# Performance work log

Measured on AMD Instinct MI355X. Metric: run time of the kernel, lower is better.

Reference implementation:

```python
import jax, jax.numpy as jnp
import numpy as np


def setup_inputs() -> dict:
    key = jax.random.key(0)
    k1, k2 = jax.random.split(key)
    B, S, H, D = 4, 2048, 12, 64
    v = jax.random.normal(k1, (B, S, H, D), dtype=jnp.float32)
    # learned per-head positional weights, sorted ascending along last dim
    # (mirrors torch.sort(torch.randn(H, S), dim=-1)[0])
    w = jnp.sort(jax.random.normal(k2, (H, S), dtype=jnp.float32), axis=-1)
    return {"v": v, "w": w}


def reference(v, w):
    # PositionalBias._naive
    # v: [B, S, H, D]; w: [H, S_max]
    B, S, H, D = v.shape
    seq_len = S - 2  # v[:, 1:-1] is the non-special-token span
    w_ = w[:, :seq_len]  # [H, seq_len]
    # _construct_bias builds bias[h, l, j] = w[h, |l - j|] (symmetric Toeplitz)
    pos = jnp.arange(seq_len)
    idx = jnp.abs(pos[:, None] - pos[None, :])  # [seq_len, seq_len]
    bias = w_[:, idx]  # [H, seq_len, seq_len]
    # zero-pad one row/col on each side -> [H, S, S]
    bias = jnp.pad(bias, ((0, 0), (1, 1), (1, 1)))
    # z_pb: [1, S, H]
    z_pb = jnp.sum(bias, axis=-1).T[None, :, :]
    # pbv: [B, S, H, D]
    pbv = jnp.einsum('nlhd,hlj->njhd', v, bias)
    return (pbv, z_pb)
```

## Files before the change

### kernel.cpp

```cpp
#include <hip/hip_runtime.h>
#include <hip/hip_bf16.h>


typedef short short8 __attribute__((ext_vector_type(8)));
typedef float floatx4 __attribute__((ext_vector_type(4)));

#define QN 4288

__device__ __attribute__((aligned(16))) short g_vt[4 * 12 * 64 * 2048];
__device__ __attribute__((aligned(16))) short g_wt[12 * QN * 8];

__device__ __forceinline__ unsigned short f2bf(float f) {
  union { __hip_bfloat16 b; unsigned short u; } cv;
  cv.b = __float2bfloat16(f);
  return cv.u;
}

__global__ __launch_bounds__(256) void prep_kernel(const float* __restrict__ v,
                                                   const float* __restrict__ w,
                                                   float* __restrict__ out) {
  __shared__ float zls[4096];
  __shared__ float wsum[4];

  const int bx  = blockIdx.x;
  const int tid = threadIdx.x;

  if (bx >= 396) {
    const int h = bx - 396;
    const float* wh = w + (size_t)h * 2048;
    short* F = g_wt + (size_t)h * QN * 8;
    for (int q = tid; q < QN; q += 256) {
      unsigned short buf[8] __attribute__((aligned(16)));
      #pragma unroll
      for (int i = 0; i < 8; ++i) {
        int t = 2174 - q - i;
        int a = t < 0 ? -t : t;
        buf[i] = (a <= 2045) ? f2bf(wh[a]) : (unsigned short)0;
      }
      *(short8*)&F[(size_t)q * 8] = *(const short8*)buf;
    }
    return;
  }

  if (bx >= 384) {
    const int h = bx - 384;
    float* wvv = zls;
    float* pfx = zls + 2048;
    const float* wh = w + (size_t)h * 2048;
    float* zout = out + 6291456;
    for (int i = tid; i < 2048; i += 256) wvv[i] = (i < 2046) ? wh[i] : 0.f;
    __syncthreads();
    const int base = tid * 8;
    float run0 = 0.f;
    #pragma unroll
    for (int k = 0; k < 8; ++k) run0 += wvv[base + k];
    float x = run0;
    #pragma unroll
    for (int dd = 1; dd < 64; dd <<= 1) {
      float y = __shfl_up(x, dd);
      if ((tid & 63) >= dd) x += y;
    }
    if ((tid & 63) == 63) wsum[tid >> 6] = x;
    __syncthreads();
    const int wid4 = tid >> 6;
    float woff = 0.f;
    #pragma unroll
    for (int u = 0; u < 3; ++u) { float t = wsum[u]; if (u < wid4) woff += t; }
    float pr = x + woff - run0;
    #pragma unroll
    for (int k = 0; k < 8; ++k) { pr += wvv[base + k]; pfx[base + k] = pr; }
    __syncthreads();
    for (int i = tid; i < 2046; i += 256) {
      float z = pfx[i] + pfx[2045 - i] - wvv[0];
      zout[(size_t)(i + 1) * 12 + h] = z;
    }
    if (tid == 0) { zout[h] = 0.f; zout[(size_t)2047 * 12 + h] = 0.f; }
    return;
  }

  const int chunk = bx & 7;
  const int slice = bx >> 3;
  const int n = slice / 12, h = slice - n * 12;
  const int lane = tid & 63;
  const int wv   = tid >> 6;
  const int l0 = chunk * 256 + wv * 64;

  const float* src = v + (((size_t)n * 2048 + l0) * 12 + h) * 64 + lane;
  short* dst = g_vt + (((size_t)n * 12 + h) * 64 + lane) * 2048 + l0;

  #pragma unroll
  for (int k = 0; k < 8; ++k) {
    float f[8];
    #pragma unroll
    for (int i = 0; i < 8; ++i) f[i] = src[(size_t)(k * 8 + i) * 768];
    short8 b;
    #pragma unroll
    for (int i = 0; i < 8; ++i) {
      int l = l0 + k * 8 + i;
      b[i] = (l == 0 || l == 2047) ? (short)0 : (short)f2bf(f[i]);
    }
    *(short8*)&dst[k * 8] = b;
  }
}

__global__ __launch_bounds__(256, 3) void gemm_kernel(float* __restrict__ out) {
  const int bx  = blockIdx.x;
  const int tid = threadIdx.x;

  const int slice = bx % 48;
  const int jt    = bx / 48;
  const int ndt = slice & 3;
  const int h   = slice >> 2;
  const int lane = tid & 63;
  const int wid  = tid >> 6;
  const int lm = lane & 15, quad = lane >> 4;
  const int jb = jt * 128;
  const int d  = wid * 16 + lm;

  const short* vtb = g_vt + (((size_t)ndt * 12 + h) * 64 + d) * 2048;
  const short* wtb = g_wt + (size_t)h * QN * 8;
  const int lane_base = 127 + quad * 8 - lm + 2047 - jb;

  auto load_af = [&](int q) -> short8 {
    return *(const short8*)&wtb[(size_t)q << 3];
  };
  auto load_bf = [&](int lb) -> short8 {
    return *(const short8*)&vtb[lb];
  };

  short8 afr[10];
  #pragma unroll
  for (int i = 0; i < 10; ++i) afr[i] = load_af((i - 7) * 16 + lane_base);
  short8 bc0 = load_bf(quad * 8);
  short8 bc1 = load_bf(32 + quad * 8);
  short8 bn0 = load_bf(64 + quad * 8);
  short8 bn1 = load_bf(96 + quad * 8);

  floatx4 acc[8];
  #pragma unroll
  for (int ma = 0; ma < 8; ++ma) acc[ma] = (floatx4){0.f, 0.f, 0.f, 0.f};

  #pragma unroll
  for (int t = 0; t < 32; ++t) {
    short8 bm0, bm1;
    if (t < 30) {
      const int lb = (t + 2) * 64 + quad * 8;
      bm0 = load_bf(lb);
      bm1 = load_bf(lb + 32);
    }
    short8 na0, na1, na2, na3;
    if (t < 31) {
      const int l0n = t * 64 + 64;
      na0 = load_af(l0n - 16 + lane_base);
      na1 = load_af(l0n      + lane_base);
      na2 = load_af(l0n + 16 + lane_base);
      na3 = load_af(l0n + 32 + lane_base);
    }

    __builtin_amdgcn_s_setprio(1);
    #pragma unroll
    for (int ma = 0; ma < 8; ++ma)
      acc[ma] = __builtin_amdgcn_mfma_f32_16x16x32_bf16(afr[7 - ma], bc0, acc[ma], 0, 0, 0);
    #pragma unroll
    for (int ma = 0; ma < 8; ++ma)
      acc[ma] = __builtin_amdgcn_mfma_f32_16x16x32_bf16(afr[9 - ma], bc1, acc[ma], 0, 0, 0);
    __builtin_amdgcn_s_setprio(0);

    if (t < 31) {
      #pragma unroll
      for (int i = 0; i < 6; ++i) afr[i] = afr[i + 4];
      afr[6] = na0; afr[7] = na1; afr[8] = na2; afr[9] = na3;
      bc0 = bn0; bc1 = bn1;
      if (t < 30) { bn0 = bm0; bn1 = bm1; }
    }
  }

  float* obase = out + (size_t)ndt * 1572864 + (size_t)h * 64 + d;
  #pragma unroll
  for (int ma = 0; ma < 8; ++ma) {
    floatx4 cc = acc[ma];
    #pragma unroll
    for (int r = 0; r < 4; ++r) {
      int j = jb + ma * 16 + quad * 4 + r;
      float val = (j == 0 || j == 2047) ? 0.f : cc[r];
      obase[(size_t)j * 768] = val;
    }
  }
}

extern "C" void kernel_launch(void* const* d_in, const int* in_sizes, int n_in,
                              void* d_out, int out_size, void* d_ws, size_t ws_size,
                              hipStream_t stream) {
  const float* v = (const float*)d_in[0];
  const float* w = (const float*)d_in[1];
  float* out = (float*)d_out;
  prep_kernel<<<dim3(408), 256, 0, stream>>>(v, w, out);
  gemm_kernel<<<dim3(768), 256, 0, stream>>>(out);
}
```

Measured before the change: 128.4 us.

## Stage Toeplitz weight band in LDS and split transpose prep into more blocks

The GEMM kernel now copies each block's 2304-entry slice of the bf16 Toeplitz weight table into shared memory once, then reads A fragments from LDS instead of global memory. The main loop is only partially unrolled, and its bounds checks become clamped indices. The prep transpose uses four times as many blocks, each handling 16 rows per wave instead of 64, to raise parallelism and memory-level concurrency. QN grows so the padded LDS window stays in bounds. The cost is an extra __syncthreads and LDS use that may limit occupancy, plus partial unrolling that may keep register rotations as real moves.

```diff
diff --git a/kernel.cpp b/kernel.cpp
--- a/kernel.cpp
+++ b/kernel.cpp
@@ -5,7 +5,7 @@
 typedef short short8 __attribute__((ext_vector_type(8)));
 typedef float floatx4 __attribute__((ext_vector_type(4)));
 
-#define QN 4288
+#define QN 4352
 
 __device__ __attribute__((aligned(16))) short g_vt[4 * 12 * 64 * 2048];
 __device__ __attribute__((aligned(16))) short g_wt[12 * QN * 8];
@@ -25,8 +25,8 @@
   const int bx  = blockIdx.x;
   const int tid = threadIdx.x;
 
-  if (bx >= 396) {
-    const int h = bx - 396;
+  if (bx >= 1548) {
+    const int h = bx - 1548;
     const float* wh = w + (size_t)h * 2048;
     short* F = g_wt + (size_t)h * QN * 8;
     for (int q = tid; q < QN; q += 256) {
@@ -42,8 +42,8 @@
     return;
   }
 
-  if (bx >= 384) {
-    const int h = bx - 384;
+  if (bx >= 1536) {
+    const int h = bx - 1536;
     float* wvv = zls;
     float* pfx = zls + 2048;
     const float* wh = w + (size_t)h * 2048;
@@ -78,32 +78,34 @@
     return;
   }
 
-  const int chunk = bx & 7;
-  const int slice = bx >> 3;
+  const int chunk = bx & 31;
+  const int slice = bx >> 5;
   const int n = slice / 12, h = slice - n * 12;
   const int lane = tid & 63;
   const int wv   = tid >> 6;
-  const int l0 = chunk * 256 + wv * 64;
+  const int l0 = chunk * 64 + wv * 16;
 
   const float* src = v + (((size_t)n * 2048 + l0) * 12 + h) * 64 + lane;
   short* dst = g_vt + (((size_t)n * 12 + h) * 64 + lane) * 2048 + l0;
 
-  #pragma unroll
-  for (int k = 0; k < 8; ++k) {
-    float f[8];
-    #pragma unroll
-    for (int i = 0; i < 8; ++i) f[i] = src[(size_t)(k * 8 + i) * 768];
+  float f[16];
+  #pragma unroll
+  for (int k = 0; k < 16; ++k) f[k] = src[(size_t)k * 768];
+  #pragma unroll
+  for (int g = 0; g < 2; ++g) {
     short8 b;
     #pragma unroll
     for (int i = 0; i < 8; ++i) {
-      int l = l0 + k * 8 + i;
-      b[i] = (l == 0 || l == 2047) ? (short)0 : (short)f2bf(f[i]);
-    }
-    *(short8*)&dst[k * 8] = b;
+      int l = l0 + g * 8 + i;
+      b[i] = (l == 0 || l == 2047) ? (short)0 : (short)f2bf(f[g * 8 + i]);
+    }
+    *(short8*)&dst[g * 8] = b;
   }
 }
 
 __global__ __launch_bounds__(256, 3) void gemm_kernel(float* __restrict__ out) {
+  __shared__ __attribute__((aligned(16))) short Als[2304 * 8];
+
   const int bx  = blockIdx.x;
   const int tid = threadIdx.x;
 
@@ -118,44 +120,48 @@
   const int d  = wid * 16 + lm;
 
   const short* vtb = g_vt + (((size_t)ndt * 12 + h) * 64 + d) * 2048;
-  const short* wtb = g_wt + (size_t)h * QN * 8;
-  const int lane_base = 127 + quad * 8 - lm + 2047 - jb;
-
-  auto load_af = [&](int q) -> short8 {
-    return *(const short8*)&wtb[(size_t)q << 3];
-  };
   auto load_bf = [&](int lb) -> short8 {
     return *(const short8*)&vtb[lb];
   };
 
-  short8 afr[10];
-  #pragma unroll
-  for (int i = 0; i < 10; ++i) afr[i] = load_af((i - 7) * 16 + lane_base);
   short8 bc0 = load_bf(quad * 8);
   short8 bc1 = load_bf(32 + quad * 8);
   short8 bn0 = load_bf(64 + quad * 8);
   short8 bn1 = load_bf(96 + quad * 8);
 
+  const short* wsrc = g_wt + (size_t)h * QN * 8 + (size_t)(2047 - jb) * 8;
+  #pragma unroll
+  for (int k = 0; k < 9; ++k) {
+    *(short8*)&Als[(size_t)(k * 256 + tid) * 8] =
+        *(const short8*)&wsrc[(size_t)(k * 256 + tid) * 8];
+  }
+  __syncthreads();
+
+  const int abase = 127 + quad * 8 - lm;
+  auto load_af = [&](int p) -> short8 {
+    return *(const short8*)&Als[(size_t)(p + abase) * 8];
+  };
+
+  short8 afr[10];
+  #pragma unroll
+  for (int i = 0; i < 10; ++i) afr[i] = load_af((i - 7) * 16);
+
   floatx4 acc[8];
   #pragma unroll
   for (int ma = 0; ma < 8; ++ma) acc[ma] = (floatx4){0.f, 0.f, 0.f, 0.f};
 
-  #pragma unroll
+  #pragma unroll 4
   for (int t = 0; t < 32; ++t) {
-    short8 bm0, bm1;
-    if (t < 30) {
-      const int lb = (t + 2) * 64 + quad * 8;
-      bm0 = load_bf(lb);
-      bm1 = load_bf(lb + 32);
-    }
-    short8 na0, na1, na2, na3;
-    if (t < 31) {
-      const int l0n = t * 64 + 64;
-      na0 = load_af(l0n - 16 + lane_base);
-      na1 = load_af(l0n      + lane_base);
-      na2 = load_af(l0n + 16 + lane_base);
-      na3 = load_af(l0n + 32 + lane_base);
-    }
+    const int l0 = t * 64;
+    int t2 = t + 2; if (t2 > 31) t2 = 31;
+    const int lb = t2 * 64 + quad * 8;
+    short8 bm0 = load_bf(lb);
+    short8 bm1 = load_bf(lb + 32);
+    const int l0n = (t < 31) ? l0 + 64 : l0;
+    short8 na0 = load_af(l0n - 16);
+    short8 na1 = load_af(l0n);
+    short8 na2 = load_af(l0n + 16);
+    short8 na3 = load_af(l0n + 32);
 
     __builtin_amdgcn_s_setprio(1);
     #pragma unroll
@@ -166,13 +172,11 @@
       acc[ma] = __builtin_amdgcn_mfma_f32_16x16x32_bf16(afr[9 - ma], bc1, acc[ma], 0, 0, 0);
     __builtin_amdgcn_s_setprio(0);
 
-    if (t < 31) {
-      #pragma unroll
-      for (int i = 0; i < 6; ++i) afr[i] = afr[i + 4];
-      afr[6] = na0; afr[7] = na1; afr[8] = na2; afr[9] = na3;
-      bc0 = bn0; bc1 = bn1;
-      if (t < 30) { bn0 = bm0; bn1 = bm1; }
-    }
+    #pragma unroll
+    for (int i = 0; i < 6; ++i) afr[i] = afr[i + 4];
+    afr[6] = na0; afr[7] = na1; afr[8] = na2; afr[9] = na3;
+    bc0 = bn0; bc1 = bn1;
+    bn0 = bm0; bn1 = bm1;
   }
 
   float* obase = out + (size_t)ndt * 1572864 + (size_t)h * 64 + d;
@@ -194,6 +198,6 @@
   const float* v = (const float*)d_in[0];
   const float* w = (const float*)d_in[1];
   float* out = (float*)d_out;
-  prep_kernel<<<dim3(408), 256, 0, stream>>>(v, w, out);
+  prep_kernel<<<dim3(1560), 256, 0, stream>>>(v, w, out);
   gemm_kernel<<<dim3(768), 256, 0, stream>>>(out);
 }
```

After: 122.1 us. -4.9%, faster.
